# Optimization experiments

Measured on AMD Instinct MI355X. Metric: run time of the kernel, lower is better.

## Reference

```python
import jax, jax.numpy as jnp
import numpy as np

# NF4 (NormalFloat4) codebook from bitsandbytes
NF4 = jnp.array([
    -1.0, -0.6961928009986877, -0.5250730514526367, -0.39491748809814453,
    -0.28444138169288635, -0.18477343022823334, -0.09105003625154495, 0.0,
    0.07958029955625534, 0.16093020141124725, 0.24611230194568634,
    0.33791524171829224, 0.44070982933044434, 0.5626170039176941,
    0.7229568362236023, 1.0], dtype=jnp.float32)

BLOCK = 64          # bnb default quantization block size
RANK = 8
ALPHA = 16
SCALING = ALPHA / RANK


def setup_inputs() -> dict:
    key = jax.random.key(0)
    k = jax.random.split(key, 6)
    B, S, I, O = 4, 2048, 4096, 4096
    x = jax.random.normal(k[0], (B, S, I), dtype=jnp.float32)
    w_codes = jax.random.randint(k[1], (O, I), 0, 16, dtype=jnp.int32)
    absmax = jax.random.uniform(k[2], (O, I // BLOCK), dtype=jnp.float32)
    bias = jax.random.normal(k[3], (O,), dtype=jnp.float32)
    lora_A = jax.random.normal(k[4], (I, RANK), dtype=jnp.float32) / np.sqrt(I)
    lora_B = jax.random.normal(k[5], (RANK, O), dtype=jnp.float32)
    return {"x": x, "w_codes": w_codes, "absmax": absmax, "bias": bias,
            "lora_A": lora_A, "lora_B": lora_B}


def reference(x, w_codes, absmax, bias, lora_A, lora_B):
    O, I = w_codes.shape
    # NF4 dequantize: code lookup scaled by per-block absmax -> W [O, I]
    W = (NF4[w_codes].reshape(O, I // BLOCK, BLOCK) * absmax[:, :, None]).reshape(O, I)
    base = jnp.einsum('bsi,oi->bso', x, W) + bias
    # low-rank LoRA branch (dropout=0 -> identity)
    lora = ((x @ lora_A) @ lora_B) * SCALING
    return base + lora
```

## Files before the change

kernel.cpp:

```cpp
#include <hip/hip_runtime.h>
#include <hip/hip_bf16.h>
#include <stdint.h>


typedef __bf16 bf16x8 __attribute__((ext_vector_type(8)));
typedef float  f32x4  __attribute__((ext_vector_type(4)));
typedef unsigned short u16x8 __attribute__((ext_vector_type(8)));

__constant__ float NF4_TAB[16] = {
    -1.0f, -0.6961928009986877f, -0.5250730514526367f, -0.39491748809814453f,
    -0.28444138169288635f, -0.18477343022823334f, -0.09105003625154495f, 0.0f,
    0.07958029955625534f, 0.16093020141124725f, 0.24611230194568634f,
    0.33791524171829224f, 0.44070982933044434f, 0.5626170039176941f,
    0.7229568362236023f, 1.0f};

__device__ __forceinline__ unsigned short f2bf(float f) {
    unsigned int u = __float_as_uint(f);
    u += 0x7FFFu + ((u >> 16) & 1u);
    return (unsigned short)(u >> 16);
}

__global__ __launch_bounds__(256) void prep_kernel(
    const float* __restrict__ x, unsigned short* __restrict__ xb, int n8, int nCvt,
    const int* __restrict__ codes, const float* __restrict__ absmax,
    const float* __restrict__ lA, const float* __restrict__ lB,
    unsigned short* __restrict__ W, int O, int I, int nIb) {
    if ((int)blockIdx.x < nCvt) {
        int i = blockIdx.x * 256 + threadIdx.x;
        if (i >= n8) return;
        const float4* p = (const float4*)x + (long)i * 2;
        float4 a = p[0], b = p[1];
        u16x8 o;
        o[0] = f2bf(a.x); o[1] = f2bf(a.y); o[2] = f2bf(a.z); o[3] = f2bf(a.w);
        o[4] = f2bf(b.x); o[5] = f2bf(b.y); o[6] = f2bf(b.z); o[7] = f2bf(b.w);
        *((u16x8*)xb + i) = o;
    } else {
        const int b2 = blockIdx.x - nCvt;
        const int o  = b2 / nIb;
        const int i0 = (b2 - o * nIb) * 2048 + threadIdx.x * 8;
        float bo[8];
#pragma unroll
        for (int r = 0; r < 8; ++r) bo[r] = lB[(long)r * O + o] * 2.0f;
        const long base = (long)o * I + i0;
        const int4* cp = (const int4*)(codes + base);
        int4 c0 = cp[0], c1 = cp[1];
        const float am = absmax[o * (I >> 6) + (i0 >> 6)];
        int cc[8] = {c0.x, c0.y, c0.z, c0.w, c1.x, c1.y, c1.z, c1.w};
        u16x8 ov;
#pragma unroll
        for (int j = 0; j < 8; ++j) {
            const float4* ap = (const float4*)(lA + (long)(i0 + j) * 8);
            float4 a0 = ap[0], a1 = ap[1];
            float w = NF4_TAB[cc[j] & 15] * am;
            w += a0.x * bo[0] + a0.y * bo[1] + a0.z * bo[2] + a0.w * bo[3]
               + a1.x * bo[4] + a1.y * bo[5] + a1.z * bo[6] + a1.w * bo[7];
            ov[j] = f2bf(w);
        }
        *(u16x8*)(W + base) = ov;
    }
}

#define BM 256
#define BN 256
#define BK 64

#define GLOAD16(g, s) __builtin_amdgcn_global_load_lds(                     \
    (const __attribute__((address_space(1))) void*)(g),                     \
    (__attribute__((address_space(3))) void*)(s), 16, 0, 0)

#define STAGE(ptr, ldsbase) do {                                            \
    GLOAD16((ptr), (char*)(ldsbase) + ldsW);                                \
    GLOAD16((ptr) + SK, (char*)(ldsbase) + 8192 + ldsW); } while (0)

#define BAR() do { asm volatile("" ::: "memory");                           \
    __builtin_amdgcn_s_barrier(); asm volatile("" ::: "memory"); } while (0)

#define MFMA_QUAD(H, KQ, BREG)                                              \
    _Pragma("unroll") for (int mi = 0; mi < 4; ++mi)                        \
    _Pragma("unroll") for (int ni = 0; ni < 2; ++ni) {                      \
        acc[H][KQ][mi][ni] = __builtin_amdgcn_mfma_f32_16x16x32_bf16(       \
            a[mi][0], BREG[ni][0], acc[H][KQ][mi][ni], 0, 0, 0);            \
        acc[H][KQ][mi][ni] = __builtin_amdgcn_mfma_f32_16x16x32_bf16(       \
            a[mi][1], BREG[ni][1], acc[H][KQ][mi][ni], 0, 0, 0); }

#define CLUSTER(H, KQ, BREG) do {                                           \
    BAR();                                                                  \
    __builtin_amdgcn_s_setprio(1);                                          \
    MFMA_QUAD(H, KQ, BREG);                                                 \
    __builtin_amdgcn_s_setprio(0);                                          \
    BAR(); } while (0)

__global__ __launch_bounds__(512, 2) void gemm_kernel(
    const unsigned short* __restrict__ A,
    const unsigned short* __restrict__ Bm,
    const float* __restrict__ bias,
    float* __restrict__ out, int M, int N, int K, int gx, int gy) {
    __shared__ char lds[2][65536];

    int bx, by;
    {
        const int bid = blockIdx.x;
        if ((gx & 7) == 0 && (gy & 7) == 0 && ((gx >> 3) * (gy >> 3)) == 8) {
            const int xcd = bid & 7, loc = bid >> 3;
            const int cxs = gx >> 3;
            const int cr = xcd / cxs, cc = xcd - cr * cxs;
            by = cr * 8 + (loc >> 3);
            bx = cc * 8 + (loc & 7);
        } else if (((gx * gy) & 7) == 0) {
            const int q = (gx * gy) >> 3;
            const int id = (bid & 7) * q + (bid >> 3);
            bx = id % gx; by = id / gx;
        } else { bx = bid % gx; by = bid / gx; }
    }

    const int t = threadIdx.x;
    const int w = t >> 6, l = t & 63;
    const int wr = w >> 2, wc = w & 3;
    const long mB = (long)by * BM;
    const long nB = (long)bx * BN;
    const int NT = K / BK;

    const int sRow = w * 8 + (l >> 3);
    const int sCol = ((l & 7) ^ (l >> 3)) << 3;
    const int ldsW = w * 1024;
    const long SK = 64L * K;
    const long HK = 128L * K;
    const unsigned short* gA = A  + (mB + sRow) * K + sCol;
    const unsigned short* gB = Bm + (nB + sRow) * K + sCol;

    const unsigned short* pA1 = gA + HK + BK;
    const unsigned short* pB1 = gB + HK + BK;
    const unsigned short* pA0 = gA + 2 * BK;
    const unsigned short* pB0 = gB + 2 * BK;

    const int fr = l & 15;
    const int aoff0 = fr * 128 + ((((l >> 4)) ^ (l & 7)) << 4);
    const int aoff1 = fr * 128 + (((4 + (l >> 4)) ^ (l & 7)) << 4);

    f32x4 acc[2][2][4][2];
#pragma unroll
    for (int h = 0; h < 2; ++h)
#pragma unroll
        for (int k = 0; k < 2; ++k)
#pragma unroll
            for (int mi = 0; mi < 4; ++mi)
#pragma unroll
                for (int ni = 0; ni < 2; ++ni)
                    acc[h][k][mi][ni] = (f32x4){0.f, 0.f, 0.f, 0.f};

    STAGE(gA,      lds[0] + 0);
    STAGE(gA + HK, lds[0] + 16384);
    STAGE(gB,      lds[0] + 32768);
    STAGE(gB + HK, lds[0] + 49152);
    STAGE(gA + BK, lds[1] + 0);
    STAGE(gB + BK, lds[1] + 32768);
    asm volatile("s_waitcnt vmcnt(4)" ::: "memory");
    BAR();

    bf16x8 a[4][2], b0[2][2], b1[2][2];

    for (int g = 0; g < NT; ++g) {
        char* cur = lds[g & 1];
        char* nxt = lds[(g & 1) ^ 1];
        const char* Ab = cur + wr * 8192;
        const char* Bb = cur + 32768 + wc * 4096;
        const bool st1 = (g + 1 < NT), st2 = (g + 2 < NT);

#pragma unroll
        for (int mi = 0; mi < 4; ++mi) {
            a[mi][0] = *(const bf16x8*)(Ab + mi * 2048 + aoff0);
            a[mi][1] = *(const bf16x8*)(Ab + mi * 2048 + aoff1);
        }
#pragma unroll
        for (int ni = 0; ni < 2; ++ni) {
            b0[ni][0] = *(const bf16x8*)(Bb + ni * 2048 + aoff0);
            b0[ni][1] = *(const bf16x8*)(Bb + ni * 2048 + aoff1);
        }
        if (st1) STAGE(pA1, nxt + 16384);
        asm volatile("s_waitcnt vmcnt(6)" ::: "memory");
        CLUSTER(0, 0, b0);

#pragma unroll
        for (int ni = 0; ni < 2; ++ni) {
            b1[ni][0] = *(const bf16x8*)(Bb + 16384 + ni * 2048 + aoff0);
            b1[ni][1] = *(const bf16x8*)(Bb + 16384 + ni * 2048 + aoff1);
        }
        if (st1) STAGE(pB1, nxt + 49152);
        CLUSTER(0, 1, b1);

#pragma unroll
        for (int mi = 0; mi < 4; ++mi) {
            a[mi][0] = *(const bf16x8*)(Ab + 16384 + mi * 2048 + aoff0);
            a[mi][1] = *(const bf16x8*)(Ab + 16384 + mi * 2048 + aoff1);
        }
        if (st2) STAGE(pA0, cur + 0);
        CLUSTER(1, 0, b0);

        if (st2) STAGE(pB0, cur + 32768);
        if (st2) { asm volatile("s_waitcnt vmcnt(8)" ::: "memory"); }
        else     { asm volatile("s_waitcnt vmcnt(0)" ::: "memory"); }
        CLUSTER(1, 1, b1);

        pA1 += BK; pB1 += BK; pA0 += BK; pB0 += BK;
    }

    const int r4 = (l >> 4) * 4;
#pragma unroll
    for (int kq = 0; kq < 2; ++kq) {
        float bs[2];
#pragma unroll
        for (int ni = 0; ni < 2; ++ni)
            bs[ni] = bias[nB + kq * 128 + wc * 32 + ni * 16 + fr];
#pragma unroll
        for (int h = 0; h < 2; ++h)
#pragma unroll
            for (int mi = 0; mi < 4; ++mi)
#pragma unroll
                for (int r = 0; r < 4; ++r) {
                    long row = mB + h * 128 + wr * 64 + mi * 16 + r4 + r;
                    float* op = out + row * N + nB + kq * 128 + wc * 32 + fr;
#pragma unroll
                    for (int ni = 0; ni < 2; ++ni)
                        op[ni * 16] = acc[h][kq][mi][ni][r] + bs[ni];
                }
    }
}

__global__ void naive_kernel(const float* __restrict__ x, const int* __restrict__ codes,
                             const float* __restrict__ absmax, const float* __restrict__ bias,
                             const float* __restrict__ lA, const float* __restrict__ lB,
                             float* __restrict__ out, int M, int I, int O) {
    long idx = (long)blockIdx.x * 256 + threadIdx.x;
    if (idx >= (long)M * O) return;
    int o = (int)(idx % O);
    long m = idx / O;
    const float* xr = x + m * I;
    const int* cr = codes + (long)o * I;
    const float* ar = absmax + (long)o * (I >> 6);
    float acc = 0.f;
    float la[8] = {0, 0, 0, 0, 0, 0, 0, 0};
    for (int i = 0; i < I; ++i) {
        float xv = xr[i];
        acc += xv * NF4_TAB[cr[i] & 15] * ar[i >> 6];
        const float* av = lA + (long)i * 8;
#pragma unroll
        for (int r = 0; r < 8; ++r) la[r] += xv * av[r];
    }
    float lv = 0.f;
#pragma unroll
    for (int r = 0; r < 8; ++r) lv += la[r] * lB[(long)r * O + o];
    out[idx] = acc + bias[o] + 2.0f * lv;
}

extern "C" void kernel_launch(void* const* d_in, const int* in_sizes, int n_in,
                              void* d_out, int out_size, void* d_ws, size_t ws_size,
                              hipStream_t stream) {
    const float* x      = (const float*)d_in[0];
    const int*   codes  = (const int*)d_in[1];
    const float* absmax = (const float*)d_in[2];
    const float* bias   = (const float*)d_in[3];
    const float* lA     = (const float*)d_in[4];
    const float* lB     = (const float*)d_in[5];
    float* out = (float*)d_out;

    const int I = in_sizes[4] / 8;
    const int O = in_sizes[3];
    const int M = in_sizes[0] / I;
    const int K = I;

    const size_t need = (size_t)M * K * 2 + (size_t)O * K * 2;
    if (ws_size < need || (M % BM) || (O % BN) || (K % 2048) || (K / BK) < 2) {
        long tot = (long)M * O;
        naive_kernel<<<(int)((tot + 255) / 256), 256, 0, stream>>>(
            x, codes, absmax, bias, lA, lB, out, M, I, O);
        return;
    }

    unsigned short* xb = (unsigned short*)d_ws;
    unsigned short* wb = xb + (size_t)M * K;

    const int n8   = (M * K) / 8;
    const int nCvt = (n8 + 255) / 256;
    const int nIb  = K / 2048;
    const int nPrep = nCvt + O * nIb;
    prep_kernel<<<nPrep, 256, 0, stream>>>(x, xb, n8, nCvt,
                                           codes, absmax, lA, lB, wb, O, K, nIb);
    const int gx = O / BN, gy = M / BM;
    gemm_kernel<<<gx * gy, 512, 0, stream>>>(xb, wb, bias, out, M, O, K, gx, gy);
}
```

Before: 364.6 us.

## Use fixed-size grid-stride prep kernel and force LDS waitcnt before MFMA clusters

The prep kernel now launches a fixed number of blocks: 4096 convert blocks and 2048 weight-build blocks. Each thread handles four strided items instead of one, which cuts block-launch and scheduling overhead and lets each thread keep several loads in flight. The weight-build path now indexes by 8-element groups across the whole matrix instead of per-row 2048-wide chunks. The GEMM's MFMA clusters now start with an explicit s_waitcnt lgkmcnt(0) and a sched_barrier, which pins instruction ordering but may reduce overlap of LDS reads with MFMAs. The fixed grid with four iterations only covers inputs up to four strides, so larger shapes would silently skip work.

```diff
diff --git a/kernel.cpp b/kernel.cpp
--- a/kernel.cpp
+++ b/kernel.cpp
@@ -20,43 +20,60 @@
     return (unsigned short)(u >> 16);
 }
 
+#define CVT_BLOCKS 4096
+#define BLD_BLOCKS 2048
+
 __global__ __launch_bounds__(256) void prep_kernel(
-    const float* __restrict__ x, unsigned short* __restrict__ xb, int n8, int nCvt,
+    const float* __restrict__ x, unsigned short* __restrict__ xb, int n8,
     const int* __restrict__ codes, const float* __restrict__ absmax,
     const float* __restrict__ lA, const float* __restrict__ lB,
-    unsigned short* __restrict__ W, int O, int I, int nIb) {
-    if ((int)blockIdx.x < nCvt) {
-        int i = blockIdx.x * 256 + threadIdx.x;
-        if (i >= n8) return;
-        const float4* p = (const float4*)x + (long)i * 2;
-        float4 a = p[0], b = p[1];
-        u16x8 o;
-        o[0] = f2bf(a.x); o[1] = f2bf(a.y); o[2] = f2bf(a.z); o[3] = f2bf(a.w);
-        o[4] = f2bf(b.x); o[5] = f2bf(b.y); o[6] = f2bf(b.z); o[7] = f2bf(b.w);
-        *((u16x8*)xb + i) = o;
+    unsigned short* __restrict__ W, int O, int I, int nW8) {
+    if ((int)blockIdx.x < CVT_BLOCKS) {
+        const int base = blockIdx.x * 256 + threadIdx.x;
+        const int stride = CVT_BLOCKS * 256;
+#pragma unroll
+        for (int k = 0; k < 4; ++k) {
+            const int i = base + k * stride;
+            if (i < n8) {
+                const float4* p = (const float4*)x + (long)i * 2;
+                float4 a = p[0], b = p[1];
+                u16x8 o;
+                o[0] = f2bf(a.x); o[1] = f2bf(a.y); o[2] = f2bf(a.z); o[3] = f2bf(a.w);
+                o[4] = f2bf(b.x); o[5] = f2bf(b.y); o[6] = f2bf(b.z); o[7] = f2bf(b.w);
+                *((u16x8*)xb + i) = o;
+            }
+        }
     } else {
-        const int b2 = blockIdx.x - nCvt;
-        const int o  = b2 / nIb;
-        const int i0 = (b2 - o * nIb) * 2048 + threadIdx.x * 8;
-        float bo[8];
-#pragma unroll
-        for (int r = 0; r < 8; ++r) bo[r] = lB[(long)r * O + o] * 2.0f;
-        const long base = (long)o * I + i0;
-        const int4* cp = (const int4*)(codes + base);
-        int4 c0 = cp[0], c1 = cp[1];
-        const float am = absmax[o * (I >> 6) + (i0 >> 6)];
-        int cc[8] = {c0.x, c0.y, c0.z, c0.w, c1.x, c1.y, c1.z, c1.w};
-        u16x8 ov;
-#pragma unroll
-        for (int j = 0; j < 8; ++j) {
-            const float4* ap = (const float4*)(lA + (long)(i0 + j) * 8);
-            float4 a0 = ap[0], a1 = ap[1];
-            float w = NF4_TAB[cc[j] & 15] * am;
-            w += a0.x * bo[0] + a0.y * bo[1] + a0.z * bo[2] + a0.w * bo[3]
-               + a1.x * bo[4] + a1.y * bo[5] + a1.z * bo[6] + a1.w * bo[7];
-            ov[j] = f2bf(w);
-        }
-        *(u16x8*)(W + base) = ov;
+        const int base = (blockIdx.x - CVT_BLOCKS) * 256 + threadIdx.x;
+        const int stride = BLD_BLOCKS * 256;
+        const int gpr = I >> 3;
+#pragma unroll
+        for (int k = 0; k < 4; ++k) {
+            const int g8 = base + k * stride;
+            if (g8 < nW8) {
+                const int o  = g8 / gpr;
+                const int i0 = (g8 - o * gpr) << 3;
+                float bo[8];
+#pragma unroll
+                for (int r = 0; r < 8; ++r) bo[r] = lB[(long)r * O + o] * 2.0f;
+                const long bse = (long)o * I + i0;
+                const int4* cp = (const int4*)(codes + bse);
+                int4 c0 = cp[0], c1 = cp[1];
+                const float am = absmax[o * (I >> 6) + (i0 >> 6)];
+                int cc[8] = {c0.x, c0.y, c0.z, c0.w, c1.x, c1.y, c1.z, c1.w};
+                u16x8 ov;
+#pragma unroll
+                for (int j = 0; j < 8; ++j) {
+                    const float4* ap = (const float4*)(lA + (long)(i0 + j) * 8);
+                    float4 a0 = ap[0], a1 = ap[1];
+                    float wv = NF4_TAB[cc[j] & 15] * am;
+                    wv += a0.x * bo[0] + a0.y * bo[1] + a0.z * bo[2] + a0.w * bo[3]
+                        + a1.x * bo[4] + a1.y * bo[5] + a1.z * bo[6] + a1.w * bo[7];
+                    ov[j] = f2bf(wv);
+                }
+                *(u16x8*)(W + bse) = ov;
+            }
+        }
     }
 }
 
@@ -85,6 +102,8 @@
 
 #define CLUSTER(H, KQ, BREG) do {                                           \
     BAR();                                                                  \
+    asm volatile("s_waitcnt lgkmcnt(0)" ::: "memory");                      \
+    __builtin_amdgcn_sched_barrier(0);                                      \
     __builtin_amdgcn_s_setprio(1);                                          \
     MFMA_QUAD(H, KQ, BREG);                                                 \
     __builtin_amdgcn_s_setprio(0);                                          \
@@ -279,12 +298,10 @@
     unsigned short* xb = (unsigned short*)d_ws;
     unsigned short* wb = xb + (size_t)M * K;
 
-    const int n8   = (M * K) / 8;
-    const int nCvt = (n8 + 255) / 256;
-    const int nIb  = K / 2048;
-    const int nPrep = nCvt + O * nIb;
-    prep_kernel<<<nPrep, 256, 0, stream>>>(x, xb, n8, nCvt,
-                                           codes, absmax, lA, lB, wb, O, K, nIb);
+    const int n8  = (M * K) / 8;
+    const int nW8 = (O * K) / 8;
+    prep_kernel<<<CVT_BLOCKS + BLD_BLOCKS, 256, 0, stream>>>(
+        x, xb, n8, codes, absmax, lA, lB, wb, O, K, nW8);
     const int gx = O / BN, gy = M / BM;
     gemm_kernel<<<gx * gy, 512, 0, stream>>>(xb, wb, bias, out, M, O, K, gx, gy);
 }
```

Measured after the change: 364.5 us. About the same (-0.0%).
